# Optimization experiments

Measured on AMD Instinct MI355X. Metric: run time of the kernel, lower is better.

Reference implementation:

```python
import jax, jax.numpy as jnp
import numpy as np

B, CIN, COUT, K = 8, 64, 64, 3
H, W = 256, 256
PAD = 1


def setup_inputs() -> dict:
    key = jax.random.key(0)
    k1, k2, k3, k4 = jax.random.split(key, 4)
    x = jax.random.normal(k1, (B, CIN, H, W), dtype=jnp.float32)
    alpha = jax.random.uniform(k2, (B, CIN, 1, 1), dtype=jnp.float32)
    # learned params per init_kwargs (groups=1 -> cin_per_group = CIN)
    weight = jax.random.normal(k3, (1, COUT, CIN, K, K), dtype=jnp.float32) * 0.05
    bias = jax.random.normal(k4, (1, COUT), dtype=jnp.float32) * 0.05
    return {"x": x, "alpha": alpha, "weight": weight, "bias": bias}


def reference(x, alpha, weight, bias):
    # cal_dim='cin': per-sample modulated weights
    # alpha: (B, CIN, 1, 1) -> (B, 1, CIN, 1, 1); weight: (1, COUT, CIN, K, K)
    w = alpha[:, None] * weight  # (B, COUT, CIN, K, K)

    def conv_one(xi, wi):
        # xi: (CIN, H, W), wi: (COUT, CIN, K, K)
        out = jax.lax.conv_general_dilated(
            xi[None], wi,
            window_strides=(1, 1),
            padding=[(PAD, PAD), (PAD, PAD)],
            dimension_numbers=("NCHW", "OIHW", "NCHW"),
        )
        return out[0]  # (COUT, H, W)

    out = jax.vmap(conv_one)(x, w)  # (B, COUT, H, W)
    # bias is repeated per-sample in the torch code -> same bias every sample
    return out + bias[0][None, :, None, None]
```

## Files before the change

kernel.cpp:

```cpp
#include <hip/hip_runtime.h>


typedef __attribute__((ext_vector_type(8))) short short8;
typedef __attribute__((ext_vector_type(4))) float float4v;

#define BB 8
#define CI_N 64
#define CO_N 64
#define HH 256
#define WW 256
#define TW 32
#define TH 8
#define HALO_W 34
#define HALO_H 10
#define HALO_PX (HALO_W * HALO_H)
#define RS 72
#define HI_OFF 32

#define NFRAG (2 * 9 * 2 * 4 * 64 * 8)

__device__ __forceinline__ unsigned f2bf(float v) {
    unsigned u = __float_as_uint(v);
    return (u + 0x7FFFu + ((u >> 16) & 1u)) >> 16;
}

__global__ void prepack_w(const float* __restrict__ w, ushort* __restrict__ wp) {
    int idx = blockIdx.x * 256 + threadIdx.x;
    if (idx >= NFRAG) return;
    int j     = idx & 7;
    int lane  = (idx >> 3) & 63;
    int mt    = (idx >> 9) & 3;
    int plane = (idx >> 11) & 1;
    int rest  = idx >> 12;
    int k     = rest % 9;
    int chunk = rest / 9;
    int co = mt * 16 + (lane & 15);
    int ci = chunk * 32 + (lane >> 4) * 8 + j;
    float v = w[(co * CI_N + ci) * 9 + k];
    unsigned hi = f2bf(v);
    float fhi = __uint_as_float(hi << 16);
    unsigned lo = f2bf(v - fhi);
    wp[idx] = (ushort)(plane ? lo : hi);
}

__global__ __launch_bounds__(512, 4) void conv_mfma(
    const float* __restrict__ x,
    const float* __restrict__ alpha,
    const ushort* __restrict__ wp,
    const float* __restrict__ bias,
    float* __restrict__ out)
{
    __shared__ __align__(16) ushort sx[HALO_PX * RS];

    const int tid    = threadIdx.x;
    const int lane   = tid & 63;
    const int w_id   = tid >> 6;
    const int n_lane = lane & 15;
    const int q      = lane >> 4;
    const int b      = blockIdx.z;
    const int gx0    = blockIdx.x * TW;
    const int gy0    = blockIdx.y * TH;
    const int m_half = w_id >> 2;
    const int n_q    = w_id & 3;

    float4v acc[2][4];
#pragma unroll
    for (int mt = 0; mt < 2; ++mt) {
        float4v bi;
#pragma unroll
        for (int r = 0; r < 4; ++r)
            bi[r] = bias[(m_half * 2 + mt) * 16 + q * 4 + r];
#pragma unroll
        for (int nt = 0; nt < 4; ++nt) acc[mt][nt] = bi;
    }

    const float* xb = x + (size_t)b * CI_N * HH * WW;
    const int vbase = (n_q * 2 * HALO_W + n_lane) * RS + q * 8;

    for (int chunk = 0; chunk < 2; ++chunk) {
        if (chunk) __syncthreads();

#pragma unroll
        for (int p = 0; p < 2; ++p) {
            const int cl = w_id * 4 + p * 2;
            const int ci = chunk * 32 + cl;
            const float a0 = alpha[b * CI_N + ci];
            const float a1 = alpha[b * CI_N + ci + 1];
            const float* xp0 = xb + (size_t)ci * HH * WW;
            const float* xp1 = xp0 + HH * WW;
#pragma unroll
            for (int it = 0; it < 6; ++it) {
                int hp = it * 64 + lane;
                if (hp < HALO_PX) {
                    int hy = hp / HALO_W;
                    int hx = hp - hy * HALO_W;
                    int gy = gy0 - 1 + hy;
                    int gx = gx0 - 1 + hx;
                    bool ok = ((unsigned)gy < HH) & ((unsigned)gx < WW);
                    int gidx = gy * WW + gx;
                    float v0 = ok ? xp0[gidx] * a0 : 0.0f;
                    float v1 = ok ? xp1[gidx] * a1 : 0.0f;
                    unsigned h0 = f2bf(v0);
                    unsigned h1 = f2bf(v1);
                    float f0 = __uint_as_float(h0 << 16);
                    float f1 = __uint_as_float(h1 << 16);
                    unsigned l0 = f2bf(v0 - f0);
                    unsigned l1 = f2bf(v1 - f1);
                    *(unsigned*)&sx[hp * RS + cl]          = h0 | (h1 << 16);
                    *(unsigned*)&sx[hp * RS + HI_OFF + cl] = l0 | (l1 << 16);
                }
            }
        }
        __syncthreads();

#pragma unroll
        for (int k = 0; k < 9; ++k) {
            const int dy = k / 3 - 1;
            const int dx = k % 3 - 1;
            short8 a_hi[2], a_lo[2];
#pragma unroll
            for (int mt = 0; mt < 2; ++mt) {
                int fh = ((chunk * 9 + k) * 2 + 0) * 4 + (m_half * 2 + mt);
                int fl = ((chunk * 9 + k) * 2 + 1) * 4 + (m_half * 2 + mt);
                a_hi[mt] = *(const short8*)(wp + (size_t)(fh * 64 + lane) * 8);
                a_lo[mt] = *(const short8*)(wp + (size_t)(fl * 64 + lane) * 8);
            }
#pragma unroll
            for (int nt_i = 0; nt_i < 4; ++nt_i) {
                const int off = ((nt_i >> 1) + 1 + dy) * HALO_W + 1 + (nt_i & 1) * 16 + dx;
                const ushort* bp = &sx[vbase + off * RS];
                short8 b_hi = *(const short8*)bp;
                short8 b_lo = *(const short8*)(bp + HI_OFF);
                acc[0][nt_i] = __builtin_amdgcn_mfma_f32_16x16x32_bf16(a_hi[0], b_hi, acc[0][nt_i], 0, 0, 0);
                acc[1][nt_i] = __builtin_amdgcn_mfma_f32_16x16x32_bf16(a_hi[1], b_hi, acc[1][nt_i], 0, 0, 0);
                acc[0][nt_i] = __builtin_amdgcn_mfma_f32_16x16x32_bf16(a_lo[0], b_hi, acc[0][nt_i], 0, 0, 0);
                acc[1][nt_i] = __builtin_amdgcn_mfma_f32_16x16x32_bf16(a_lo[1], b_hi, acc[1][nt_i], 0, 0, 0);
                acc[0][nt_i] = __builtin_amdgcn_mfma_f32_16x16x32_bf16(a_hi[0], b_lo, acc[0][nt_i], 0, 0, 0);
                acc[1][nt_i] = __builtin_amdgcn_mfma_f32_16x16x32_bf16(a_hi[1], b_lo, acc[1][nt_i], 0, 0, 0);
            }
        }
    }

#pragma unroll
    for (int mt = 0; mt < 2; ++mt) {
        const int m0 = (m_half * 2 + mt) * 16;
#pragma unroll
        for (int nt_i = 0; nt_i < 4; ++nt_i) {
            const int nt = n_q * 4 + nt_i;
            const int gy = gy0 + (nt >> 1);
            const int gx = gx0 + (nt & 1) * 16 + n_lane;
#pragma unroll
            for (int r = 0; r < 4; ++r) {
                const int co = m0 + q * 4 + r;
                out[(((size_t)b * CO_N + co) * HH + gy) * WW + gx] = acc[mt][nt_i][r];
            }
        }
    }
}

extern "C" void kernel_launch(void* const* d_in, const int* in_sizes, int n_in,
                              void* d_out, int out_size, void* d_ws, size_t ws_size,
                              hipStream_t stream) {
    const float* x     = (const float*)d_in[0];
    const float* alpha = (const float*)d_in[1];
    const float* w     = (const float*)d_in[2];
    const float* bias  = (const float*)d_in[3];
    float* out  = (float*)d_out;
    ushort* wpk = (ushort*)d_ws;

    prepack_w<<<dim3((NFRAG + 255) / 256), dim3(256), 0, stream>>>(w, wpk);

    dim3 grid(WW / TW, HH / TH, BB);
    conv_mfma<<<grid, dim3(512), 0, stream>>>(x, alpha, wpk, bias, out);
}
```

Measured before the change: 370.9 us.

## Prepack input into padded channel-last bf16 hi/lo layout before the MFMA conv

Adds a pre-pass that scales x by alpha, splits each value into bf16 hi/lo parts and writes them to a zero-bordered, channel-last workspace buffer. The conv kernel then fills shared memory with contiguous 16-byte loads into an XOR-swizzled layout, with no bounds checks or conversion math, and asks for higher occupancy in its launch bounds. The aim is to remove the per-block strided fp32 gathers and repeated conversion work from the conv's load phase. The cost is an extra full read and write of the input through global memory plus two more launches. The old kernel is kept as a fallback when the workspace is too small.

```diff
diff --git a/kernel.cpp b/kernel.cpp
--- a/kernel.cpp
+++ b/kernel.cpp
@@ -14,10 +14,16 @@
 #define HALO_W 34
 #define HALO_H 10
 #define HALO_PX (HALO_W * HALO_H)
-#define RS 72
-#define HI_OFF 32
-
+
+#define GP 258
+#define XROW_US (GP * 64)
+#define XB_US   ((size_t)GP * XROW_US)
 #define NFRAG (2 * 9 * 2 * 4 * 64 * 8)
+#define XQ_OFF_US ((size_t)NFRAG)
+#define XQ_US   (16 * XB_US)
+#define WS_NEED ((XQ_OFF_US + XQ_US) * 2)
+
+#define SX_US (HALO_PX * 64)
 
 __device__ __forceinline__ unsigned f2bf(float v) {
     unsigned u = __float_as_uint(v);
@@ -43,14 +49,74 @@
     wp[idx] = (ushort)(plane ? lo : hi);
 }
 
-__global__ __launch_bounds__(512, 4) void conv_mfma(
-    const float* __restrict__ x,
-    const float* __restrict__ alpha,
+__global__ void zero_border(ushort* __restrict__ xq) {
+    int g = blockIdx.x * 256 + threadIdx.x;
+    if (g >= 131584) return;
+    int slot = g & 7;
+    int rest = g >> 3;
+    int c  = rest % 1028;
+    int cb = rest / 1028;
+    int gy, gx;
+    if (c < 258)      { gy = 0;   gx = c; }
+    else if (c < 516) { gy = 257; gx = c - 258; }
+    else { int r = c - 516; gy = 1 + (r >> 1); gx = (r & 1) ? 257 : 0; }
+    size_t us = (size_t)cb * XB_US + (size_t)gy * XROW_US + (size_t)gx * 64 + slot * 8;
+    short8 z = {0, 0, 0, 0, 0, 0, 0, 0};
+    *(short8*)(xq + us) = z;
+}
+
+__global__ __launch_bounds__(256) void prepack_x(
+    const float* __restrict__ x, const float* __restrict__ alpha,
+    ushort* __restrict__ xq)
+{
+    __shared__ float sxT[32][65];
+    __shared__ float sa[64];
+    const int t = threadIdx.x;
+    const int b = blockIdx.x >> 8;
+    const int y = blockIdx.x & 255;
+    if (t < 64) sa[t] = alpha[b * CI_N + t];
+    const float* xb = x + (size_t)b * CI_N * HH * WW + (size_t)y * WW;
+    const int lx = t >> 2, plane = (t >> 1) & 1, jh = t & 1;
+    __syncthreads();
+#pragma unroll 1
+    for (int tile = 0; tile < 8; ++tile) {
+        const int xt = tile >> 1, chunk = tile & 1;
+#pragma unroll
+        for (int it = 0; it < 8; ++it) {
+            int cil = it * 4 + (t >> 6);
+            int ci  = chunk * 32 + cil;
+            int xx  = xt * 64 + (t & 63);
+            sxT[cil][t & 63] = xb[(size_t)ci * (HH * WW) + xx] * sa[ci];
+        }
+        __syncthreads();
+        unsigned pk[8];
+#pragma unroll
+        for (int jj = 0; jj < 16; jj += 2) {
+            float v0 = sxT[jh * 16 + jj][lx];
+            float v1 = sxT[jh * 16 + jj + 1][lx];
+            unsigned h0 = f2bf(v0), h1 = f2bf(v1);
+            unsigned o0 = h0, o1 = h1;
+            if (plane) {
+                o0 = f2bf(v0 - __uint_as_float(h0 << 16));
+                o1 = f2bf(v1 - __uint_as_float(h1 << 16));
+            }
+            pk[jj >> 1] = o0 | (o1 << 16);
+        }
+        size_t us = (size_t)(chunk * 8 + b) * XB_US + (size_t)(y + 1) * XROW_US
+                  + (size_t)(xt * 64 + lx + 1) * 64 + plane * 32 + jh * 16;
+        *(uint4*)(xq + us)     = make_uint4(pk[0], pk[1], pk[2], pk[3]);
+        *(uint4*)(xq + us + 8) = make_uint4(pk[4], pk[5], pk[6], pk[7]);
+        __syncthreads();
+    }
+}
+
+__global__ __launch_bounds__(512, 6) void conv_mfma(
+    const ushort* __restrict__ xq,
     const ushort* __restrict__ wp,
     const float* __restrict__ bias,
     float* __restrict__ out)
 {
-    __shared__ __align__(16) ushort sx[HALO_PX * RS];
+    __shared__ __align__(16) ushort sx[SX_US];
 
     const int tid    = threadIdx.x;
     const int lane   = tid & 63;
@@ -74,12 +140,116 @@
         for (int nt = 0; nt < 4; ++nt) acc[mt][nt] = bi;
     }
 
-    const float* xb = x + (size_t)b * CI_N * HH * WW;
-    const int vbase = (n_q * 2 * HALO_W + n_lane) * RS + q * 8;
-
     for (int chunk = 0; chunk < 2; ++chunk) {
         if (chunk) __syncthreads();
 
+        short8 stg[6];
+        int    lofs[6];
+#pragma unroll
+        for (int it = 0; it < 6; ++it) {
+            int li = it * 512 + tid;
+            if (li < SX_US / 8) {
+                int px = li >> 3;
+                int sl = li & 7;
+                int hy = px / HALO_W;
+                int hx = px - hy * HALO_W;
+                size_t g = (size_t)(chunk * 8 + b) * XB_US
+                         + (size_t)(gy0 + hy) * XROW_US
+                         + (size_t)(gx0 + hx) * 64 + sl * 8;
+                stg[it]  = *(const short8*)(xq + g);
+                lofs[it] = px * 64 + ((sl ^ (px & 7)) << 3);
+            }
+        }
+#pragma unroll
+        for (int it = 0; it < 6; ++it) {
+            int li = it * 512 + tid;
+            if (li < SX_US / 8) *(short8*)&sx[lofs[it]] = stg[it];
+        }
+        __syncthreads();
+
+#pragma unroll
+        for (int k = 0; k < 9; ++k) {
+            const int dy = k / 3 - 1;
+            const int dx = k % 3 - 1;
+            short8 a_hi[2], a_lo[2];
+#pragma unroll
+            for (int mt = 0; mt < 2; ++mt) {
+                int fh = ((chunk * 9 + k) * 2 + 0) * 4 + (m_half * 2 + mt);
+                int fl = ((chunk * 9 + k) * 2 + 1) * 4 + (m_half * 2 + mt);
+                a_hi[mt] = *(const short8*)(wp + (size_t)(fh * 64 + lane) * 8);
+                a_lo[mt] = *(const short8*)(wp + (size_t)(fl * 64 + lane) * 8);
+            }
+#pragma unroll
+            for (int nt_i = 0; nt_i < 4; ++nt_i) {
+                const int prow = n_q * 2 + (nt_i >> 1) + 1 + dy;
+                const int px   = prow * HALO_W + (nt_i & 1) * 16 + 1 + dx + n_lane;
+                const int sw   = (q ^ (px & 7)) << 3;
+                short8 b_hi = *(const short8*)&sx[px * 64 + sw];
+                short8 b_lo = *(const short8*)&sx[px * 64 + (sw ^ 32)];
+                acc[0][nt_i] = __builtin_amdgcn_mfma_f32_16x16x32_bf16(a_hi[0], b_hi, acc[0][nt_i], 0, 0, 0);
+                acc[1][nt_i] = __builtin_amdgcn_mfma_f32_16x16x32_bf16(a_hi[1], b_hi, acc[1][nt_i], 0, 0, 0);
+                acc[0][nt_i] = __builtin_amdgcn_mfma_f32_16x16x32_bf16(a_lo[0], b_hi, acc[0][nt_i], 0, 0, 0);
+                acc[1][nt_i] = __builtin_amdgcn_mfma_f32_16x16x32_bf16(a_lo[1], b_hi, acc[1][nt_i], 0, 0, 0);
+                acc[0][nt_i] = __builtin_amdgcn_mfma_f32_16x16x32_bf16(a_hi[0], b_lo, acc[0][nt_i], 0, 0, 0);
+                acc[1][nt_i] = __builtin_amdgcn_mfma_f32_16x16x32_bf16(a_hi[1], b_lo, acc[1][nt_i], 0, 0, 0);
+            }
+        }
+    }
+
+#pragma unroll
+    for (int mt = 0; mt < 2; ++mt) {
+        const int m0 = (m_half * 2 + mt) * 16;
+#pragma unroll
+        for (int nt_i = 0; nt_i < 4; ++nt_i) {
+            const int nt = n_q * 4 + nt_i;
+            const int gy = gy0 + (nt >> 1);
+            const int gx = gx0 + (nt & 1) * 16 + n_lane;
+#pragma unroll
+            for (int r = 0; r < 4; ++r) {
+                const int co = m0 + q * 4 + r;
+                out[(((size_t)b * CO_N + co) * HH + gy) * WW + gx] = acc[mt][nt_i][r];
+            }
+        }
+    }
+}
+
+#define RS_FB 72
+#define HI_OFF_FB 32
+
+__global__ __launch_bounds__(512, 4) void conv_mfma_fb(
+    const float* __restrict__ x, const float* __restrict__ alpha,
+    const ushort* __restrict__ wp, const float* __restrict__ bias,
+    float* __restrict__ out)
+{
+    __shared__ __align__(16) ushort sx[HALO_PX * RS_FB];
+
+    const int tid    = threadIdx.x;
+    const int lane   = tid & 63;
+    const int w_id   = tid >> 6;
+    const int n_lane = lane & 15;
+    const int q      = lane >> 4;
+    const int b      = blockIdx.z;
+    const int gx0    = blockIdx.x * TW;
+    const int gy0    = blockIdx.y * TH;
+    const int m_half = w_id >> 2;
+    const int n_q    = w_id & 3;
+
+    float4v acc[2][4];
+#pragma unroll
+    for (int mt = 0; mt < 2; ++mt) {
+        float4v bi;
+#pragma unroll
+        for (int r = 0; r < 4; ++r)
+            bi[r] = bias[(m_half * 2 + mt) * 16 + q * 4 + r];
+#pragma unroll
+        for (int nt = 0; nt < 4; ++nt) acc[mt][nt] = bi;
+    }
+
+    const float* xb = x + (size_t)b * CI_N * HH * WW;
+    const int vbase = (n_q * 2 * HALO_W + n_lane) * RS_FB + q * 8;
+
+    for (int chunk = 0; chunk < 2; ++chunk) {
+        if (chunk) __syncthreads();
 #pragma unroll
         for (int p = 0; p < 2; ++p) {
             const int cl = w_id * 4 + p * 2;
@@ -106,13 +276,12 @@
                     float f1 = __uint_as_float(h1 << 16);
                     unsigned l0 = f2bf(v0 - f0);
                     unsigned l1 = f2bf(v1 - f1);
-                    *(unsigned*)&sx[hp * RS + cl]          = h0 | (h1 << 16);
-                    *(unsigned*)&sx[hp * RS + HI_OFF + cl] = l0 | (l1 << 16);
+                    *(unsigned*)&sx[hp * RS_FB + cl]             = h0 | (h1 << 16);
+                    *(unsigned*)&sx[hp * RS_FB + HI_OFF_FB + cl] = l0 | (l1 << 16);
                 }
             }
         }
         __syncthreads();
-
 #pragma unroll
         for (int k = 0; k < 9; ++k) {
             const int dy = k / 3 - 1;
@@ -128,9 +297,9 @@
 #pragma unroll
             for (int nt_i = 0; nt_i < 4; ++nt_i) {
                 const int off = ((nt_i >> 1) + 1 + dy) * HALO_W + 1 + (nt_i & 1) * 16 + dx;
-                const ushort* bp = &sx[vbase + off * RS];
+                const ushort* bp = &sx[vbase + off * RS_FB];
                 short8 b_hi = *(const short8*)bp;
-                short8 b_lo = *(const short8*)(bp + HI_OFF);
+                short8 b_lo = *(const short8*)(bp + HI_OFF_FB);
                 acc[0][nt_i] = __builtin_amdgcn_mfma_f32_16x16x32_bf16(a_hi[0], b_hi, acc[0][nt_i], 0, 0, 0);
                 acc[1][nt_i] = __builtin_amdgcn_mfma_f32_16x16x32_bf16(a_hi[1], b_hi, acc[1][nt_i], 0, 0, 0);
                 acc[0][nt_i] = __builtin_amdgcn_mfma_f32_16x16x32_bf16(a_lo[0], b_hi, acc[0][nt_i], 0, 0, 0);
@@ -169,7 +338,14 @@
     ushort* wpk = (ushort*)d_ws;
 
     prepack_w<<<dim3((NFRAG + 255) / 256), dim3(256), 0, stream>>>(w, wpk);
-
     dim3 grid(WW / TW, HH / TH, BB);
-    conv_mfma<<<grid, dim3(512), 0, stream>>>(x, alpha, wpk, bias, out);
-}
+
+    if (ws_size >= WS_NEED) {
+        ushort* xq = wpk + XQ_OFF_US;
+        zero_border<<<dim3(514), dim3(256), 0, stream>>>(xq);
+        prepack_x<<<dim3(BB * HH), dim3(256), 0, stream>>>(x, alpha, xq);
+        conv_mfma<<<grid, dim3(512), 0, stream>>>(xq, wpk, bias, out);
+    } else {
+        conv_mfma_fb<<<grid, dim3(512), 0, stream>>>(x, alpha, wpk, bias, out);
+    }
+}
```

New measurement: 954.3 us. 157% more time.

## Swizzle shared halo layout and stage 8 channels per thread with vector stores

Applied to the files above, without the earlier changes.

Replaces the padded row-stride shared-memory layout with a dense 64-ushort-per-pixel layout that uses an XOR swizzle on the 8-channel group index, so hi and lo planes fall in distinct bank groups. The staging loop now has each thread load 8 channels for one pixel and write them as 16-byte vector stores, where before it packed 2 channels into 4-byte stores. This is meant to cut LDS bank conflicts on both the writes and the MFMA operand reads, and to reduce the number of store instructions. In exchange, each thread keeps 8 global loads in flight, which raises register pressure, and the loads are clamped to offset 0 for out-of-bounds halo pixels.

```diff
diff --git a/kernel.cpp b/kernel.cpp
--- a/kernel.cpp
+++ b/kernel.cpp
@@ -14,10 +14,9 @@
 #define HALO_W 34
 #define HALO_H 10
 #define HALO_PX (HALO_W * HALO_H)
-#define RS 72
-#define HI_OFF 32
 
 #define NFRAG (2 * 9 * 2 * 4 * 64 * 8)
+#define SX_US (HALO_PX * 64)
 
 __device__ __forceinline__ unsigned f2bf(float v) {
     unsigned u = __float_as_uint(v);
@@ -50,7 +49,7 @@
     const float* __restrict__ bias,
     float* __restrict__ out)
 {
-    __shared__ __align__(16) ushort sx[HALO_PX * RS];
+    __shared__ __align__(16) ushort sx[SX_US];
 
     const int tid    = threadIdx.x;
     const int lane   = tid & 63;
@@ -75,40 +74,44 @@
     }
 
     const float* xb = x + (size_t)b * CI_N * HH * WW;
-    const int vbase = (n_q * 2 * HALO_W + n_lane) * RS + q * 8;
 
     for (int chunk = 0; chunk < 2; ++chunk) {
         if (chunk) __syncthreads();
 
 #pragma unroll
-        for (int p = 0; p < 2; ++p) {
-            const int cl = w_id * 4 + p * 2;
-            const int ci = chunk * 32 + cl;
-            const float a0 = alpha[b * CI_N + ci];
-            const float a1 = alpha[b * CI_N + ci + 1];
-            const float* xp0 = xb + (size_t)ci * HH * WW;
-            const float* xp1 = xp0 + HH * WW;
+        for (int it = 0; it < 3; ++it) {
+            const int g  = it * 8 + w_id;
+            const int s  = g / 6;
+            const int gi = g - s * 6;
+            const int px = gi * 64 + lane;
+            if (px < HALO_PX) {
+                const int hy = px / HALO_W;
+                const int hx = px - hy * HALO_W;
+                const int gy = gy0 - 1 + hy;
+                const int gx = gx0 - 1 + hx;
+                const bool ok = ((unsigned)gy < HH) & ((unsigned)gx < WW);
+                const int gofs = ok ? gy * WW + gx : 0;
+                const int ci0 = chunk * 32 + s * 8;
+                const float* xp = xb + (size_t)ci0 * (HH * WW) + gofs;
+                float v[8];
 #pragma unroll
-            for (int it = 0; it < 6; ++it) {
-                int hp = it * 64 + lane;
-                if (hp < HALO_PX) {
-                    int hy = hp / HALO_W;
-                    int hx = hp - hy * HALO_W;
-                    int gy = gy0 - 1 + hy;
-                    int gx = gx0 - 1 + hx;
-                    bool ok = ((unsigned)gy < HH) & ((unsigned)gx < WW);
-                    int gidx = gy * WW + gx;
-                    float v0 = ok ? xp0[gidx] * a0 : 0.0f;
-                    float v1 = ok ? xp1[gidx] * a1 : 0.0f;
-                    unsigned h0 = f2bf(v0);
-                    unsigned h1 = f2bf(v1);
-                    float f0 = __uint_as_float(h0 << 16);
-                    float f1 = __uint_as_float(h1 << 16);
-                    unsigned l0 = f2bf(v0 - f0);
-                    unsigned l1 = f2bf(v1 - f1);
-                    *(unsigned*)&sx[hp * RS + cl]          = h0 | (h1 << 16);
-                    *(unsigned*)&sx[hp * RS + HI_OFF + cl] = l0 | (l1 << 16);
+                for (int c = 0; c < 8; ++c) {
+                    float t = xp[c * (HH * WW)] * alpha[b * CI_N + ci0 + c];
+                    v[c] = ok ? t : 0.0f;
                 }
+                unsigned ph[4], pl[4];
+#pragma unroll
+                for (int j = 0; j < 4; ++j) {
+                    unsigned h0 = f2bf(v[2 * j]);
+                    unsigned h1 = f2bf(v[2 * j + 1]);
+                    unsigned l0 = f2bf(v[2 * j]     - __uint_as_float(h0 << 16));
+                    unsigned l1 = f2bf(v[2 * j + 1] - __uint_as_float(h1 << 16));
+                    ph[j] = h0 | (h1 << 16);
+                    pl[j] = l0 | (l1 << 16);
+                }
+                const int off = px * 64 + ((s ^ (px & 7)) << 3);
+                *(uint4*)&sx[off]      = make_uint4(ph[0], ph[1], ph[2], ph[3]);
+                *(uint4*)&sx[off ^ 32] = make_uint4(pl[0], pl[1], pl[2], pl[3]);
             }
         }
         __syncthreads();
@@ -127,10 +130,11 @@
             }
 #pragma unroll
             for (int nt_i = 0; nt_i < 4; ++nt_i) {
-                const int off = ((nt_i >> 1) + 1 + dy) * HALO_W + 1 + (nt_i & 1) * 16 + dx;
-                const ushort* bp = &sx[vbase + off * RS];
-                short8 b_hi = *(const short8*)bp;
-                short8 b_lo = *(const short8*)(bp + HI_OFF);
+                const int prow = n_q * 2 + (nt_i >> 1) + 1 + dy;
+                const int px   = prow * HALO_W + (nt_i & 1) * 16 + 1 + dx + n_lane;
+                const int sw   = (q ^ (px & 7)) << 3;
+                short8 b_hi = *(const short8*)&sx[px * 64 + sw];
+                short8 b_lo = *(const short8*)&sx[px * 64 + (sw ^ 32)];
                 acc[0][nt_i] = __builtin_amdgcn_mfma_f32_16x16x32_bf16(a_hi[0], b_hi, acc[0][nt_i], 0, 0, 0);
                 acc[1][nt_i] = __builtin_amdgcn_mfma_f32_16x16x32_bf16(a_hi[1], b_hi, acc[1][nt_i], 0, 0, 0);
                 acc[0][nt_i] = __builtin_amdgcn_mfma_f32_16x16x32_bf16(a_lo[0], b_hi, acc[0][nt_i], 0, 0, 0);
```

Result: slower. 409.3 us (+10.4%).
